# Performance work log

Hardware: AMD Instinct MI355X
Metric: run time of the kernel (lower is better)

Reference implementation:

```python
import jax, jax.numpy as jnp
import numpy as np

V, T, D, H, DK = 16, 2048, 64, 128, 48
LONGEST_GAP, TIME_WINDOW = 144, 48
N_ROLE = 2 * V * V + V


def _run_lengths(md):
    Tn = md.shape[-1]
    m = np.stack((md, md[:, ::-1]), 0).astype(np.int64)
    m[:, :, 0] = 1 - m[:, :, 0]
    for i in range(Tn - 1):
        m[:, :, i + 1] = (1 - m[:, :, i + 1]) * (1 + m[:, :, i])
    return m[0], m[1][:, ::-1].copy()


def _tree_depth_np(mask, times):
    # faithful numpy port of the cached branch of _compute_tree_depth
    Vn, Tn = mask.shape
    time_ind = np.argsort(times, axis=-1)
    time_rev = np.argsort(time_ind, axis=-1)
    mask_depth = np.take_along_axis(mask.astype(np.int64), time_ind, -1)
    current_depth = 1
    max_depth = np.zeros_like(mask_depth)
    prev_mask = np.zeros_like(max_depth)
    next_mask = np.zeros_like(max_depth)
    prev_values = np.zeros_like(max_depth)
    next_values = np.zeros_like(max_depth)
    mask_depth_copy = mask_depth.copy()
    mask_l, mask_r = _run_lengths(mask_depth)
    ci = np.tile(np.arange(Tn), (Vn, 1))
    max_ind = Tn - 1
    while (mask_l + mask_r - 1).max() > LONGEST_GAP:
        centers = mask_l == LONGEST_GAP
        left_ind = mask_l >= LONGEST_GAP
        right_ind = (mask_r + mask_l - 1 >= LONGEST_GAP) & (mask_l <= LONGEST_GAP)
        next_mask[centers] = ((ci + mask_r) > max_ind)[centers].astype(np.int64)
        prev_values[centers] = ci[centers] - mask_l[centers]
        next_values[centers] = (ci[centers] + mask_r[centers]) * (1 - next_mask[centers])
        current_depth += 1
        current_val = mask_l + mask_r
        mask_l[left_ind] -= LONGEST_GAP
        mask_r[right_ind] -= (current_val - LONGEST_GAP)[right_ind]
        mask_r[centers] = 0
        mask_depth_copy[centers] = 1
    mask_depth = mask_depth_copy
    if (1 - mask_depth[:, -1]).sum() > 0 or (1 - mask_depth[:, 0]).sum() > 0:
        end_indices = mask_depth[:, -1] == 0
        start_indices = mask_depth[:, 0] == 0
        prev_mask[:, 0] = start_indices
        next_mask[:, -1] = end_indices
        first_hist = np.arange(Tn, 0, -1)
        last_hist = np.arange(Tn)
        first_hist = np.argmax(first_hist[None, :] * mask_depth, -1)
        last_hist = np.argmax(last_hist[None, :] * mask_depth, -1)
        next_values[start_indices, 0] = first_hist[start_indices]
        prev_values[end_indices, -1] = last_hist[end_indices]
        mask_depth[:, 0] = 1
        mask_depth[:, -1] = 1
        max_depth[end_indices, -1] += current_depth
        max_depth[start_indices, 0] += current_depth
        current_depth += 1
    mask_l, mask_r = _run_lengths(mask_depth)
    while mask_l.sum() > 0:
        half = (mask_l + mask_r) // 2
        centers = (half == mask_l) & (half > 0)
        max_depth[centers] += current_depth
        prev_values[centers] = ci[centers] - mask_l[centers]
        next_values[centers] = ci[centers] + mask_r[centers]
        current_depth += 1
        odd = (mask_l + mask_r + 1) % 2
        s1 = mask_l >= half
        mask_l[s1] -= half[s1]
        s2 = (mask_r > half - odd) & (half > 0)
        mask_r[s2] -= (half - odd)[s2] + 1
    window_indices = ci - TIME_WINDOW
    window_mask = (window_indices < 0) | (window_indices > max_ind)
    window_mask[:, TIME_WINDOW:] |= max_depth[:, TIME_WINDOW:] > max_depth[:, :-TIME_WINDOW]
    window_mask = window_mask.astype(np.int64)
    window_indices = np.clip(window_indices, 0, max_ind)
    max_depth_f = np.take_along_axis(max_depth, time_rev, -1).astype(np.float32)
    next_mask_f = np.take_along_axis(next_mask, time_rev, -1).astype(np.float32)
    prev_mask_f = np.take_along_axis(prev_mask, time_rev, -1).astype(np.float32)
    window_mask_f = np.take_along_axis(window_mask, time_rev, -1).astype(np.float32)
    pv = np.take_along_axis(time_ind, np.clip(prev_values, 0, max_ind), -1)
    pv = np.take_along_axis(pv, time_rev, -1)
    nv = np.take_along_axis(time_ind, np.clip(next_values, 0, max_ind), -1)
    nv = np.take_along_axis(nv, time_rev, -1)
    wi = np.take_along_axis(time_ind, window_indices, -1)
    wi = np.take_along_axis(wi, time_rev, -1)
    offsets = Tn * np.arange(Vn)[:, None]
    indices = np.arange(Tn)[None, :] + offsets
    pv = pv + offsets
    nv = nv + offsets
    wi = wi + offsets
    max_depth_f = max_depth_f + time_ind / 2.0 / (2.0 * Tn)
    return dict(max_depth=max_depth_f, prev_values=pv, next_values=nv, indices=indices,
                prev_mask=prev_mask_f, next_mask=next_mask_f, window_indices=wi,
                window_mask=window_mask_f)


def _mlp(x, W1, b1, W2, b2):
    return jax.nn.relu(x @ W1 + b1) @ W2 + b2


def _forward(encoded, u, Wq1, bq1, Wq2, bq2, Wk1, bk1, Wk2, bk2, Wv1, bv1, Wv2, bv2,
             role_emb, Wd1, bd1, Wd2, bd2, Wm1, bm1, Wm2, bm2,
             prev_values, next_values, window_indices, indices,
             prev_mask, next_mask, window_mask, max_depth):
    Vn, Tn = max_depth.shape
    N = Vn * Tn
    enc = encoded[0].reshape(N, -1)  # [N, D]
    uv = u[0].reshape(N)
    # per-forward depth jitter (torch: max_depth += rand_like/2/(2T))
    md = max_depth + jax.random.uniform(jax.random.key(42), max_depth.shape, max_depth.dtype) / (4.0 * Tn)
    comp = md[:, :, None] > md.T[None]  # [V, T, V]: query deeper than key -> key conditioned on
    pv = jnp.broadcast_to(prev_values.T[None], (Vn, Tn, Vn))
    nv = jnp.where(comp, indices.T[None], next_values.T[None])
    base = Vn * jnp.arange(Vn, dtype=jnp.int32)[:, None] + jnp.arange(Vn, dtype=jnp.int32)[None, :]
    prev_role = jnp.broadcast_to(base[:, None, :], (Vn, Tn, Vn))
    next_role = Vn * Vn + prev_role
    window_role = 2 * Vn * Vn + jnp.broadcast_to(jnp.arange(Vn, dtype=jnp.int32)[:, None, None], (Vn, Tn, 1))
    valid_prev = jnp.broadcast_to((prev_mask.T == 0.0)[None], (Vn, Tn, Vn))
    valid_next = jnp.logical_or(comp, (next_mask.T == 0.0)[None])
    valid_win = (window_mask == 0.0)[:, :, None]
    K = 2 * Vn + 1
    nbr = jnp.concatenate([pv, nv, window_indices[:, :, None]], -1).reshape(N, K)
    roles = jnp.concatenate([prev_role, next_role, window_role], -1).reshape(N, K)
    valid = jnp.concatenate([valid_prev, valid_next, valid_win], -1).reshape(N, K)
    q = _mlp(enc, Wq1, bq1, Wq2, bq2)  # [N, DK]
    k = _mlp(enc, Wk1, bk1, Wk2, bk2)
    v = _mlp(enc, Wv1, bv1, Wv2, bv2)
    keys = k[nbr] + role_emb[roles]  # [N, K, DK] irregular gather
    vals = v[nbr]
    scores = jnp.einsum('nd,nkd->nk', q, keys) / jnp.sqrt(jnp.asarray(q.shape[-1], q.dtype))
    attn = jax.nn.softmax(jnp.where(valid, scores, -1e9), axis=-1)
    ctx = jnp.einsum('nk,nkd->nd', attn, vals)
    dp = _mlp(jnp.concatenate([enc, ctx], -1), Wd1, bd1, Wd2, bd2)  # copula dist params
    mp = _mlp(enc, Wm1, bm1, Wm2, bm2)  # marginal params

    def nlogp(x, mu, log_s):
        s = jax.nn.softplus(log_s) + 1e-3
        z = (x - mu) / s
        return 0.5 * z * z + jnp.log(s) + 0.5 * jnp.log(2.0 * jnp.pi)

    nll = nlogp(uv, dp[:, 0], dp[:, 1]) + nlogp(uv, mp[:, 0], mp[:, 1])
    return nll.reshape(Vn, Tn)


def setup_inputs() -> dict:
    rng = np.random.default_rng(0)
    times = np.sort(rng.uniform(size=(V, T)).astype(np.float32), axis=-1)
    mask = np.zeros((V, T), dtype=bool)
    mask[:, : T // 2] = True  # observed history / prediction gap > longest_gap
    c = _tree_depth_np(mask, times)
    key = jax.random.key(0)
    ks = jax.random.split(key, 13)

    def lin(k, din, dout):
        return jax.random.normal(k, (din, dout), jnp.float32) / np.sqrt(din)

    return {
        'encoded': jax.random.normal(ks[0], (1, V, T, D), jnp.float32),
        'u': jax.random.uniform(ks[1], (1, V, T), jnp.float32),
        'Wq1': lin(ks[2], D, H), 'bq1': jnp.zeros(H, jnp.float32),
        'Wq2': lin(ks[3], H, DK), 'bq2': jnp.zeros(DK, jnp.float32),
        'Wk1': lin(ks[4], D, H), 'bk1': jnp.zeros(H, jnp.float32),
        'Wk2': lin(ks[5], H, DK), 'bk2': jnp.zeros(DK, jnp.float32),
        'Wv1': lin(ks[6], D, H), 'bv1': jnp.zeros(H, jnp.float32),
        'Wv2': lin(ks[7], H, DK), 'bv2': jnp.zeros(DK, jnp.float32),
        'role_emb': 0.02 * jax.random.normal(ks[8], (N_ROLE, DK), jnp.float32),
        'Wd1': lin(ks[9], D + DK, H), 'bd1': jnp.zeros(H, jnp.float32),
        'Wd2': lin(ks[10], H, 2), 'bd2': jnp.zeros(2, jnp.float32),
        'Wm1': lin(ks[11], D, H), 'bm1': jnp.zeros(H, jnp.float32),
        'Wm2': lin(ks[12], H, 2), 'bm2': jnp.zeros(2, jnp.float32),
        'prev_values': jnp.asarray(c['prev_values'], jnp.int32),
        'next_values': jnp.asarray(c['next_values'], jnp.int32),
        'window_indices': jnp.asarray(c['window_indices'], jnp.int32),
        'indices': jnp.asarray(c['indices'], jnp.int32),
        'prev_mask': jnp.asarray(c['prev_mask'], jnp.float32),
        'next_mask': jnp.asarray(c['next_mask'], jnp.float32),
        'window_mask': jnp.asarray(c['window_mask'], jnp.float32),
        'max_depth': jnp.asarray(c['max_depth'], jnp.float32),
    }


def reference(encoded, u, Wq1, bq1, Wq2, bq2, Wk1, bk1, Wk2, bk2, Wv1, bv1, Wv2, bv2,
              role_emb, Wd1, bd1, Wd2, bd2, Wm1, bm1, Wm2, bm2,
              prev_values, next_values, window_indices, indices,
              prev_mask, next_mask, window_mask, max_depth):
    return _forward(encoded, u, Wq1, bq1, Wq2, bq2, Wk1, bk1, Wk2, bk2, Wv1, bv1, Wv2, bv2,
                    role_emb, Wd1, bd1, Wd2, bd2, Wm1, bm1, Wm2, bm2,
                    prev_values, next_values, window_indices, indices,
                    prev_mask, next_mask, window_mask, max_depth)
```

## Files before the change

### kernel.cpp

```cpp
#include <hip/hip_runtime.h>
#include <math.h>

#define VN 16
#define TN 2048
#define NROWS (VN*TN)
#define DIN 64
#define HID 128
#define DKD 48
#define KNB 33
#define BR64 64
#define BRH 32
#define KPAD 52
#define XPAD 68
#define HPAD 66
#define XPADH 36

__device__ __forceinline__ unsigned rotl32(unsigned x, int d){ return (x<<d)|(x>>(32-d)); }

__device__ __forceinline__ void tf2x32(unsigned c0, unsigned c1, unsigned& y0, unsigned& y1){
  const unsigned k0 = 0u, k1 = 42u;
  const unsigned k2 = k0 ^ k1 ^ 0x1BD11BDAu;
  unsigned x0 = c0, x1 = c1;
  x0 += k0; x1 += k1;
#define TF_R(r) { x0 += x1; x1 = rotl32(x1,(r)); x1 ^= x0; }
  TF_R(13) TF_R(15) TF_R(26) TF_R(6)   x0 += k1; x1 += k2 + 1u;
  TF_R(17) TF_R(29) TF_R(16) TF_R(24)  x0 += k2; x1 += k0 + 2u;
  TF_R(13) TF_R(15) TF_R(26) TF_R(6)   x0 += k0; x1 += k1 + 3u;
  TF_R(17) TF_R(29) TF_R(16) TF_R(24)  x0 += k1; x1 += k2 + 4u;
  TF_R(13) TF_R(15) TF_R(26) TF_R(6)   x0 += k2; x1 += k0 + 5u;
#undef TF_R
  y0 = x0; y1 = x1;
}

__device__ __forceinline__ double md64_of(const float* __restrict__ max_depth, int n){
  unsigned y0, y1;
  tf2x32(0u, (unsigned)n, y0, y1);
  unsigned long long bits = (((unsigned long long)y0) << 32) | (unsigned long long)y1;
  unsigned long long fb = (bits >> 12) | 0x3FF0000000000000ull;
  double f; __builtin_memcpy(&f, &fb, 8);
  f -= 1.0;
  return (double)max_depth[n] + f * (1.0/8192.0);
}

__global__ __launch_bounds__(256) void prep_kernel(const float* __restrict__ max_depth,
    const int* __restrict__ pv, const int* __restrict__ nv,
    const float* __restrict__ pm, const float* __restrict__ nm,
    double* __restrict__ mdT, int* __restrict__ pvT, int* __restrict__ nvT,
    float* __restrict__ pmT, float* __restrict__ nmT)
{
  int n = blockIdx.x*256 + threadIdx.x;
  int v = n >> 11, t = n & 2047;
  int o = t*VN + v;
  mdT[o]  = md64_of(max_depth, n);
  pvT[o]  = pv[n];
  nvT[o]  = nv[n];
  pmT[o]  = pm[n];
  nmT[o]  = nm[n];
}

__global__ __launch_bounds__(256) void qkv_kernel(const float* __restrict__ enc,
    const float* __restrict__ Wq1, const float* __restrict__ bq1,
    const float* __restrict__ Wq2, const float* __restrict__ bq2,
    const float* __restrict__ Wk1, const float* __restrict__ bk1,
    const float* __restrict__ Wk2, const float* __restrict__ bk2,
    const float* __restrict__ Wv1, const float* __restrict__ bv1,
    const float* __restrict__ Wv2, const float* __restrict__ bv2,
    float* __restrict__ qo, float* __restrict__ ko, float* __restrict__ vo)
{
  __shared__ __align__(16) float s_x[DIN][XPAD];
  __shared__ __align__(16) float s_h[HID][HPAD];
  int tid = threadIdx.x;
  int mm   = blockIdx.x / 512;
  int base = (blockIdx.x - mm*512) * BR64;

  const float *W1, *b1, *W2, *b2; float* outp;
  if (mm == 0){ W1=Wq1; b1=bq1; W2=Wq2; b2=bq2; outp=qo; }
  else if (mm == 1){ W1=Wk1; b1=bk1; W2=Wk2; b2=bk2; outp=ko; }
  else        { W1=Wv1; b1=bv1; W2=Wv2; b2=bv2; outp=vo; }

  for (int idx = tid; idx < BR64*DIN; idx += 256){
    int r = idx >> 6, c = idx & 63;
    s_x[c][r] = enc[(size_t)(base+r)*DIN + c];
  }
  __syncthreads();

  const int u0 = (tid & 31) * 4;
  const int r0 = (tid >> 5) * 8;
  {
    float acc[8][4];
    float c0=b1[u0], c1=b1[u0+1], c2=b1[u0+2], c3=b1[u0+3];
    #pragma unroll
    for (int r=0;r<8;r++){ acc[r][0]=c0; acc[r][1]=c1; acc[r][2]=c2; acc[r][3]=c3; }
    #pragma unroll 8
    for (int i=0;i<DIN;i++){
      const float4 xa = *reinterpret_cast<const float4*>(&s_x[i][r0]);
      const float4 xb = *reinterpret_cast<const float4*>(&s_x[i][r0+4]);
      const float4 wv = *reinterpret_cast<const float4*>(&W1[i*HID + u0]);
      float xd[8] = {xa.x, xa.y, xa.z, xa.w, xb.x, xb.y, xb.z, xb.w};
      float wd[4] = {wv.x, wv.y, wv.z, wv.w};
      #pragma unroll
      for (int r=0;r<8;r++)
        #pragma unroll
        for (int j=0;j<4;j++)
          acc[r][j] = fmaf(xd[r], wd[j], acc[r][j]);
    }
    #pragma unroll
    for (int j=0;j<4;j++){
      float4 h0, h1;
      h0.x=fmaxf(acc[0][j],0.0f); h0.y=fmaxf(acc[1][j],0.0f);
      h0.z=fmaxf(acc[2][j],0.0f); h0.w=fmaxf(acc[3][j],0.0f);
      h1.x=fmaxf(acc[4][j],0.0f); h1.y=fmaxf(acc[5][j],0.0f);
      h1.z=fmaxf(acc[6][j],0.0f); h1.w=fmaxf(acc[7][j],0.0f);
      *reinterpret_cast<float4*>(&s_h[u0+j][r0])   = h0;
      *reinterpret_cast<float4*>(&s_h[u0+j][r0+4]) = h1;
    }
  }
  __syncthreads();

  const int uo0 = (tid & 15) * 3;
  const int rr0 = (tid >> 4) * 4;
  {
    float a[4][3];
    float c0=b2[uo0], c1=b2[uo0+1], c2=b2[uo0+2];
    #pragma unroll
    for (int r=0;r<4;r++){ a[r][0]=c0; a[r][1]=c1; a[r][2]=c2; }
    #pragma unroll 8
    for (int i=0;i<HID;i++){
      const float4 hv = *reinterpret_cast<const float4*>(&s_h[i][rr0]);
      float w0 = W2[i*DKD+uo0], w1 = W2[i*DKD+uo0+1], w2 = W2[i*DKD+uo0+2];
      float hd[4] = {hv.x, hv.y, hv.z, hv.w};
      #pragma unroll
      for (int r=0;r<4;r++){
        a[r][0]=fmaf(hd[r],w0,a[r][0]);
        a[r][1]=fmaf(hd[r],w1,a[r][1]);
        a[r][2]=fmaf(hd[r],w2,a[r][2]);
      }
    }
    #pragma unroll
    for (int r=0;r<4;r++){
      float* op = outp + (size_t)(base+rr0+r)*DKD;
      op[uo0]=a[r][0]; op[uo0+1]=a[r][1]; op[uo0+2]=a[r][2];
    }
  }
}

__global__ __launch_bounds__(256) void attn_kernel(const float* __restrict__ qv,
    const float* __restrict__ kv, const float* __restrict__ vv,
    const float* __restrict__ role_emb, const double* __restrict__ mdT,
    const int* __restrict__ pvT, const int* __restrict__ nvT,
    const float* __restrict__ pmT, const float* __restrict__ nmT,
    const int* __restrict__ window_indices, const float* __restrict__ window_mask,
    float* __restrict__ ctx_out)
{
  __shared__ __align__(16) float s_role[KNB][KPAD];
  __shared__ __align__(16) float s_q[8][DKD];
  __shared__ float s_p[8][KNB];
  __shared__ int   s_idx[8][KNB];
  int tid  = threadIdx.x;
  int wid  = tid >> 6;
  int lane = tid & 63;
  int nb = blockIdx.x*8;
  int n0 = nb + wid*2;
  int vrow = n0 >> 11;
  int t0   = n0 & 2047;

  for (int idx = tid; idx < 8*DKD; idx += 256){
    int r = idx / DKD, d = idx - r*DKD;
    s_q[r][d] = qv[(size_t)(nb+r)*DKD + d];
  }
  for (int idx = tid; idx < KNB*DKD; idx += 256){
    int j = idx / DKD, d = idx - j*DKD;
    int role = (j < 16) ? (vrow<<4)+j : ((j < 32) ? 256+(vrow<<4)+(j-16) : 512+vrow);
    s_role[j][d] = role_emb[(size_t)role*DKD + d];
  }
  __syncthreads();

  float sc0 = -INFINITY, sc1 = -INFINITY;
  if (lane < KNB){
    int g0, g1; bool va0, va1;
    if (lane < 16){
      int o0 = t0*VN + lane, o1 = o0 + VN;
      g0 = pvT[o0];            g1 = pvT[o1];
      va0 = (pmT[o0] == 0.0f); va1 = (pmT[o1] == 0.0f);
    } else if (lane < 32){
      int v2 = lane - 16;
      int o0 = t0*VN + v2, o1 = o0 + VN;
      bool c0 = mdT[t0*VN + vrow]     > mdT[o0];
      bool c1 = mdT[(t0+1)*VN + vrow] > mdT[o1];
      g0 = c0 ? (v2*TN + t0)     : nvT[o0];
      g1 = c1 ? (v2*TN + t0 + 1) : nvT[o1];
      va0 = c0 || (nmT[o0] == 0.0f);
      va1 = c1 || (nmT[o1] == 0.0f);
    } else {
      g0 = window_indices[n0];   g1 = window_indices[n0+1];
      va0 = (window_mask[n0] == 0.0f); va1 = (window_mask[n0+1] == 0.0f);
    }
    s_idx[wid*2  ][lane] = g0;
    s_idx[wid*2+1][lane] = g1;
    const float4* kp0 = reinterpret_cast<const float4*>(kv + (size_t)g0*DKD);
    const float4* kp1 = reinterpret_cast<const float4*>(kv + (size_t)g1*DKD);
    float a0 = 0.0f, a1 = 0.0f;
    #pragma unroll
    for (int d4 = 0; d4 < DKD/4; d4++){
      const float4 rr = *reinterpret_cast<const float4*>(&s_role[lane][4*d4]);
      const float4 q0 = *reinterpret_cast<const float4*>(&s_q[wid*2  ][4*d4]);
      const float4 q1 = *reinterpret_cast<const float4*>(&s_q[wid*2+1][4*d4]);
      const float4 k0 = kp0[d4];
      const float4 k1 = kp1[d4];
      a0 = fmaf(q0.x, k0.x + rr.x, a0); a1 = fmaf(q1.x, k1.x + rr.x, a1);
      a0 = fmaf(q0.y, k0.y + rr.y, a0); a1 = fmaf(q1.y, k1.y + rr.y, a1);
      a0 = fmaf(q0.z, k0.z + rr.z, a0); a1 = fmaf(q1.z, k1.z + rr.z, a1);
      a0 = fmaf(q0.w, k0.w + rr.w, a0); a1 = fmaf(q1.w, k1.w + rr.w, a1);
    }
    sc0 = a0 / 6.928203230275509f;
    sc1 = a1 / 6.928203230275509f;
    if (!va0) sc0 = -1e9f;
    if (!va1) sc1 = -1e9f;
  }
  float m0 = sc0, m1 = sc1;
  #pragma unroll
  for (int o=32;o>0;o>>=1){
    m0 = fmaxf(m0, __shfl_xor(m0, o, 64));
    m1 = fmaxf(m1, __shfl_xor(m1, o, 64));
  }
  float e0 = (lane < KNB) ? expf(sc0 - m0) : 0.0f;
  float e1 = (lane < KNB) ? expf(sc1 - m1) : 0.0f;
  float s0 = e0, s1 = e1;
  #pragma unroll
  for (int o=32;o>0;o>>=1){
    s0 += __shfl_xor(s0, o, 64);
    s1 += __shfl_xor(s1, o, 64);
  }
  if (lane < KNB){
    s_p[wid*2  ][lane] = e0 / s0;
    s_p[wid*2+1][lane] = e1 / s1;
  }

  if (lane < DKD){
    float c0 = 0.0f, c1 = 0.0f;
    #pragma unroll 8
    for (int j=0;j<KNB;j++){
      int i0 = __builtin_amdgcn_readfirstlane(s_idx[wid*2  ][j]);
      int i1 = __builtin_amdgcn_readfirstlane(s_idx[wid*2+1][j]);
      c0 = fmaf(s_p[wid*2  ][j], vv[(size_t)i0*DKD + lane], c0);
      c1 = fmaf(s_p[wid*2+1][j], vv[(size_t)i1*DKD + lane], c1);
    }
    ctx_out[(size_t)n0*DKD + lane]       = c0;
    ctx_out[(size_t)(n0+1)*DKD + lane]   = c1;
  }
}

__device__ __forceinline__ double nlogp_d(double x, double mu, double ls){
  double sp = fmax(ls, 0.0) + log1p(exp(-fabs(ls)));
  double s = sp + 1e-3;
  double z = (x - mu) / s;
  return 0.5*z*z + log(s) + 0.9189385332046727417803297;
}

__global__ __launch_bounds__(256) void heads_kernel(const float* __restrict__ enc,
    const float* __restrict__ ctx, const float* __restrict__ uu,
    const float* __restrict__ Wd1, const float* __restrict__ bd1,
    const float* __restrict__ Wd2, const float* __restrict__ bd2,
    const float* __restrict__ Wm1, const float* __restrict__ bm1,
    const float* __restrict__ Wm2, const float* __restrict__ bm2,
    float* __restrict__ out)
{
  __shared__ __align__(16) float s_x[DIN+DKD][XPADH];
  __shared__ float s_o[BRH][4];
  int tid = threadIdx.x;
  int base = blockIdx.x * BRH;

  for (int idx = tid; idx < BRH*DIN; idx += 256){
    int r = idx >> 6, c = idx & 63;
    s_x[c][r] = enc[(size_t)(base+r)*DIN + c];
  }
  for (int idx = tid; idx < BRH*DKD; idx += 256){
    int r = idx / DKD, c = idx - r*DKD;
    s_x[DIN + c][r] = ctx[(size_t)(base+r)*DKD + c];
  }
  __syncthreads();

  const int u0 = (tid & 31) * 4;
  const int r0 = (tid >> 5) * 4;

  float pd[4][2] = {{0,0},{0,0},{0,0},{0,0}};
  float pm[4][2] = {{0,0},{0,0},{0,0},{0,0}};

  {
    float acc[4][4];
    float c0=bd1[u0], c1=bd1[u0+1], c2=bd1[u0+2], c3=bd1[u0+3];
    #pragma unroll
    for (int r=0;r<4;r++){ acc[r][0]=c0; acc[r][1]=c1; acc[r][2]=c2; acc[r][3]=c3; }
    #pragma unroll 8
    for (int i=0;i<DIN+DKD;i++){
      const float4 xv = *reinterpret_cast<const float4*>(&s_x[i][r0]);
      const float4 wv = *reinterpret_cast<const float4*>(&Wd1[i*HID + u0]);
      float xd[4] = {xv.x, xv.y, xv.z, xv.w};
      float wd[4] = {wv.x, wv.y, wv.z, wv.w};
      #pragma unroll
      for (int r=0;r<4;r++)
        #pragma unroll
        for (int j=0;j<4;j++)
          acc[r][j] = fmaf(xd[r], wd[j], acc[r][j]);
    }
    #pragma unroll
    for (int j=0;j<4;j++){
      const float2 w2 = *reinterpret_cast<const float2*>(&Wd2[(u0+j)*2]);
      #pragma unroll
      for (int r=0;r<4;r++){
        float h = fmaxf(acc[r][j], 0.0f);
        pd[r][0] = fmaf(h, w2.x, pd[r][0]);
        pd[r][1] = fmaf(h, w2.y, pd[r][1]);
      }
    }
  }
  {
    float acc[4][4];
    float c0=bm1[u0], c1=bm1[u0+1], c2=bm1[u0+2], c3=bm1[u0+3];
    #pragma unroll
    for (int r=0;r<4;r++){ acc[r][0]=c0; acc[r][1]=c1; acc[r][2]=c2; acc[r][3]=c3; }
    #pragma unroll 8
    for (int i=0;i<DIN;i++){
      const float4 xv = *reinterpret_cast<const float4*>(&s_x[i][r0]);
      const float4 wv = *reinterpret_cast<const float4*>(&Wm1[i*HID + u0]);
      float xd[4] = {xv.x, xv.y, xv.z, xv.w};
      float wd[4] = {wv.x, wv.y, wv.z, wv.w};
      #pragma unroll
      for (int r=0;r<4;r++)
        #pragma unroll
        for (int j=0;j<4;j++)
          acc[r][j] = fmaf(xd[r], wd[j], acc[r][j]);
    }
    #pragma unroll
    for (int j=0;j<4;j++){
      const float2 w2 = *reinterpret_cast<const float2*>(&Wm2[(u0+j)*2]);
      #pragma unroll
      for (int r=0;r<4;r++){
        float h = fmaxf(acc[r][j], 0.0f);
        pm[r][0] = fmaf(h, w2.x, pm[r][0]);
        pm[r][1] = fmaf(h, w2.y, pm[r][1]);
      }
    }
  }
  #pragma unroll
  for (int o=1;o<=16;o<<=1){
    #pragma unroll
    for (int r=0;r<4;r++){
      pd[r][0]+=__shfl_xor(pd[r][0],o,64); pd[r][1]+=__shfl_xor(pd[r][1],o,64);
      pm[r][0]+=__shfl_xor(pm[r][0],o,64); pm[r][1]+=__shfl_xor(pm[r][1],o,64);
    }
  }
  if ((tid & 31) == 0){
    #pragma unroll
    for (int r=0;r<4;r++){
      s_o[r0+r][0] = pd[r][0] + bd2[0];
      s_o[r0+r][1] = pd[r][1] + bd2[1];
      s_o[r0+r][2] = pm[r][0] + bm2[0];
      s_o[r0+r][3] = pm[r][1] + bm2[1];
    }
  }
  __syncthreads();

  if (tid < BRH){
    double x = (double)uu[base + tid];
    out[base + tid] = (float)(nlogp_d(x, (double)s_o[tid][0], (double)s_o[tid][1]) +
                              nlogp_d(x, (double)s_o[tid][2], (double)s_o[tid][3]));
  }
}

extern "C" void kernel_launch(void* const* d_in, const int* in_sizes, int n_in,
                              void* d_out, int out_size, void* d_ws, size_t ws_size,
                              hipStream_t stream) {
  const float* encoded = (const float*)d_in[0];
  const float* u       = (const float*)d_in[1];
  const float* Wq1 = (const float*)d_in[2];  const float* bq1 = (const float*)d_in[3];
  const float* Wq2 = (const float*)d_in[4];  const float* bq2 = (const float*)d_in[5];
  const float* Wk1 = (const float*)d_in[6];  const float* bk1 = (const float*)d_in[7];
  const float* Wk2 = (const float*)d_in[8];  const float* bk2 = (const float*)d_in[9];
  const float* Wv1 = (const float*)d_in[10]; const float* bv1 = (const float*)d_in[11];
  const float* Wv2 = (const float*)d_in[12]; const float* bv2 = (const float*)d_in[13];
  const float* role_emb = (const float*)d_in[14];
  const float* Wd1 = (const float*)d_in[15]; const float* bd1 = (const float*)d_in[16];
  const float* Wd2 = (const float*)d_in[17]; const float* bd2 = (const float*)d_in[18];
  const float* Wm1 = (const float*)d_in[19]; const float* bm1 = (const float*)d_in[20];
  const float* Wm2 = (const float*)d_in[21]; const float* bm2 = (const float*)d_in[22];
  const int*   prev_values    = (const int*)d_in[23];
  const int*   next_values    = (const int*)d_in[24];
  const int*   window_indices = (const int*)d_in[25];
  const float* prev_mask   = (const float*)d_in[27];
  const float* next_mask   = (const float*)d_in[28];
  const float* window_mask = (const float*)d_in[29];
  const float* max_depth   = (const float*)d_in[30];
  float* out = (float*)d_out;

  double* mdT = (double*)d_ws;
  float* q  = (float*)(mdT + NROWS);
  float* k  = q  + (size_t)NROWS*DKD;
  float* v  = k  + (size_t)NROWS*DKD;
  float* cx = v  + (size_t)NROWS*DKD;
  int*   pvT  = (int*)(cx + (size_t)NROWS*DKD);
  int*   nvT  = pvT + NROWS;
  float* pmT  = (float*)(nvT + NROWS);
  float* nmT  = pmT + NROWS;

  prep_kernel<<<NROWS/256, 256, 0, stream>>>(max_depth,
      prev_values, next_values, prev_mask, next_mask,
      mdT, pvT, nvT, pmT, nmT);
  qkv_kernel<<<3*(NROWS/BR64), 256, 0, stream>>>(encoded,
      Wq1,bq1,Wq2,bq2, Wk1,bk1,Wk2,bk2, Wv1,bv1,Wv2,bv2, q, k, v);
  attn_kernel<<<NROWS/8, 256, 0, stream>>>(q, k, v, role_emb, mdT,
      pvT, nvT, pmT, nmT, window_indices, window_mask, cx);
  heads_kernel<<<NROWS/BRH, 256, 0, stream>>>(encoded, cx, u,
      Wd1,bd1,Wd2,bd2, Wm1,bm1,Wm2,bm2, out);
}
```

Before: 139.5 us.

## Restructure attention per timestep with shared K/V gather and precomputed role-query scores

Attention now runs one block per timestep covering all 16 vertices. The 64 distinct neighbour K/V rows are gathered once into shared memory and reused across vertices, instead of each row pair independently gathering 33 K and V rows from global memory. The role-embedding dot products q·role are split out into a separate rq_kernel, and window indices and masks are transposed in the prep kernel. This removes redundant global gathers at the cost of an extra kernel launch and an extra intermediate buffer.

Result: no change. 138.5 us (-0.8%).

```diff
diff --git a/kernel.cpp b/kernel.cpp
--- a/kernel.cpp
+++ b/kernel.cpp
@@ -10,10 +10,11 @@
 #define KNB 33
 #define BR64 64
 #define BRH 32
-#define KPAD 52
 #define XPAD 68
 #define HPAD 66
 #define XPADH 36
+#define SPAD 52
+#define RQW 528
 
 __device__ __forceinline__ unsigned rotl32(unsigned x, int d){ return (x<<d)|(x>>(32-d)); }
 
@@ -45,8 +46,10 @@
 __global__ __launch_bounds__(256) void prep_kernel(const float* __restrict__ max_depth,
     const int* __restrict__ pv, const int* __restrict__ nv,
     const float* __restrict__ pm, const float* __restrict__ nm,
+    const int* __restrict__ wi, const float* __restrict__ wm,
     double* __restrict__ mdT, int* __restrict__ pvT, int* __restrict__ nvT,
-    float* __restrict__ pmT, float* __restrict__ nmT)
+    float* __restrict__ pmT, float* __restrict__ nmT,
+    int* __restrict__ wiT, float* __restrict__ wmT)
 {
   int n = blockIdx.x*256 + threadIdx.x;
   int v = n >> 11, t = n & 2047;
@@ -56,6 +59,46 @@
   nvT[o]  = nv[n];
   pmT[o]  = pm[n];
   nmT[o]  = nm[n];
+  wiT[o]  = wi[n];
+  wmT[o]  = wm[n];
+}
+
+__global__ __launch_bounds__(256) void rq_kernel(const float* __restrict__ q,
+    const float* __restrict__ role_emb, float* __restrict__ rqT)
+{
+  __shared__ __align__(16) float s_R[KNB][SPAD];
+  __shared__ __align__(16) float s_Q[64][SPAD];
+  int tid = threadIdx.x;
+  int v  = blockIdx.x >> 5;
+  int tc = blockIdx.x & 31;
+  int t0 = tc*64;
+
+  for (int idx = tid; idx < KNB*DKD; idx += 256){
+    int j = idx / DKD, d = idx - j*DKD;
+    int role = (j<16) ? (v*16+j) : ((j<32) ? 256+v*16+(j-16) : 512+v);
+    s_R[j][d] = role_emb[(size_t)role*DKD + d];
+  }
+  for (int idx = tid; idx < 64*DKD; idx += 256){
+    int r = idx / DKD, d = idx - r*DKD;
+    s_Q[r][d] = q[((size_t)v*TN + t0 + r)*DKD + d];
+  }
+  __syncthreads();
+
+  int r = tid & 63, p = tid >> 6;
+  int t = t0 + r;
+  for (int j = p; j < KNB; j += 4){
+    float acc = 0.0f;
+    #pragma unroll
+    for (int d4=0; d4<12; d4++){
+      const float4 qq = *reinterpret_cast<const float4*>(&s_Q[r][4*d4]);
+      const float4 rr = *reinterpret_cast<const float4*>(&s_R[j][4*d4]);
+      acc = fmaf(qq.x, rr.x, acc);
+      acc = fmaf(qq.y, rr.y, acc);
+      acc = fmaf(qq.z, rr.z, acc);
+      acc = fmaf(qq.w, rr.w, acc);
+    }
+    rqT[(size_t)t*RQW + v*KNB + j] = acc;
+  }
 }
 
 __global__ __launch_bounds__(256) void qkv_kernel(const float* __restrict__ enc,
@@ -146,107 +189,128 @@
 
 __global__ __launch_bounds__(256) void attn_kernel(const float* __restrict__ qv,
     const float* __restrict__ kv, const float* __restrict__ vv,
-    const float* __restrict__ role_emb, const double* __restrict__ mdT,
+    const double* __restrict__ mdT,
     const int* __restrict__ pvT, const int* __restrict__ nvT,
     const float* __restrict__ pmT, const float* __restrict__ nmT,
-    const int* __restrict__ window_indices, const float* __restrict__ window_mask,
+    const int* __restrict__ wiT, const float* __restrict__ wmT,
+    const float* __restrict__ rqT,
     float* __restrict__ ctx_out)
 {
-  __shared__ __align__(16) float s_role[KNB][KPAD];
-  __shared__ __align__(16) float s_q[8][DKD];
-  __shared__ float s_p[8][KNB];
-  __shared__ int   s_idx[8][KNB];
-  int tid  = threadIdx.x;
-  int wid  = tid >> 6;
-  int lane = tid & 63;
-  int nb = blockIdx.x*8;
-  int n0 = nb + wid*2;
-  int vrow = n0 >> 11;
-  int t0   = n0 & 2047;
-
-  for (int idx = tid; idx < 8*DKD; idx += 256){
-    int r = idx / DKD, d = idx - r*DKD;
-    s_q[r][d] = qv[(size_t)(nb+r)*DKD + d];
-  }
-  for (int idx = tid; idx < KNB*DKD; idx += 256){
-    int j = idx / DKD, d = idx - j*DKD;
-    int role = (j < 16) ? (vrow<<4)+j : ((j < 32) ? 256+(vrow<<4)+(j-16) : 512+vrow);
-    s_role[j][d] = role_emb[(size_t)role*DKD + d];
-  }
-  __syncthreads();
-
-  float sc0 = -INFINITY, sc1 = -INFINITY;
-  if (lane < KNB){
-    int g0, g1; bool va0, va1;
-    if (lane < 16){
-      int o0 = t0*VN + lane, o1 = o0 + VN;
-      g0 = pvT[o0];            g1 = pvT[o1];
-      va0 = (pmT[o0] == 0.0f); va1 = (pmT[o1] == 0.0f);
-    } else if (lane < 32){
-      int v2 = lane - 16;
-      int o0 = t0*VN + v2, o1 = o0 + VN;
-      bool c0 = mdT[t0*VN + vrow]     > mdT[o0];
-      bool c1 = mdT[(t0+1)*VN + vrow] > mdT[o1];
-      g0 = c0 ? (v2*TN + t0)     : nvT[o0];
-      g1 = c1 ? (v2*TN + t0 + 1) : nvT[o1];
-      va0 = c0 || (nmT[o0] == 0.0f);
-      va1 = c1 || (nmT[o1] == 0.0f);
-    } else {
-      g0 = window_indices[n0];   g1 = window_indices[n0+1];
-      va0 = (window_mask[n0] == 0.0f); va1 = (window_mask[n0+1] == 0.0f);
-    }
-    s_idx[wid*2  ][lane] = g0;
-    s_idx[wid*2+1][lane] = g1;
-    const float4* kp0 = reinterpret_cast<const float4*>(kv + (size_t)g0*DKD);
-    const float4* kp1 = reinterpret_cast<const float4*>(kv + (size_t)g1*DKD);
-    float a0 = 0.0f, a1 = 0.0f;
-    #pragma unroll
-    for (int d4 = 0; d4 < DKD/4; d4++){
-      const float4 rr = *reinterpret_cast<const float4*>(&s_role[lane][4*d4]);
-      const float4 q0 = *reinterpret_cast<const float4*>(&s_q[wid*2  ][4*d4]);
-      const float4 q1 = *reinterpret_cast<const float4*>(&s_q[wid*2+1][4*d4]);
-      const float4 k0 = kp0[d4];
-      const float4 k1 = kp1[d4];
-      a0 = fmaf(q0.x, k0.x + rr.x, a0); a1 = fmaf(q1.x, k1.x + rr.x, a1);
-      a0 = fmaf(q0.y, k0.y + rr.y, a0); a1 = fmaf(q1.y, k1.y + rr.y, a1);
-      a0 = fmaf(q0.z, k0.z + rr.z, a0); a1 = fmaf(q1.z, k1.z + rr.z, a1);
-      a0 = fmaf(q0.w, k0.w + rr.w, a0); a1 = fmaf(q1.w, k1.w + rr.w, a1);
-    }
-    sc0 = a0 / 6.928203230275509f;
-    sc1 = a1 / 6.928203230275509f;
-    if (!va0) sc0 = -1e9f;
-    if (!va1) sc1 = -1e9f;
-  }
-  float m0 = sc0, m1 = sc1;
+  __shared__ __align__(16) float s_K[64][SPAD];
+  __shared__ __align__(16) float s_V[64][SPAD];
+  __shared__ __align__(16) float s_Q[16][SPAD];
+  __shared__ float s_rq[16][34];
+  __shared__ int    s_g[64];
+  __shared__ double s_md[16];
+  __shared__ float  s_pm[16], s_nm[16], s_wm[16];
+  __shared__ float  s_P1[16][17], s_P2i[16][17], s_P2n[16][17], s_pw[16];
+
+  int tid = threadIdx.x;
+  int t = blockIdx.x;
+  int mbase = t*VN;
+
+  if (tid < 64){
+    int c = tid & 15, g;
+    if (tid < 16)      g = pvT[mbase + c];
+    else if (tid < 32) g = c*TN + t;
+    else if (tid < 48) g = nvT[mbase + c];
+    else               g = wiT[mbase + c];
+    s_g[tid] = g;
+  } else if (tid < 80){
+    s_md[tid-64] = mdT[mbase + (tid-64)];
+  } else if (tid < 96){
+    s_pm[tid-80] = pmT[mbase + (tid-80)];
+  } else if (tid < 112){
+    s_nm[tid-96] = nmT[mbase + (tid-96)];
+  } else if (tid < 128){
+    s_wm[tid-112] = wmT[mbase + (tid-112)];
+  }
+  for (int idx = tid; idx < 16*DKD; idx += 256){
+    int v = idx / DKD, d = idx - v*DKD;
+    s_Q[v][d] = qv[((size_t)v*TN + t)*DKD + d];
+  }
+  for (int idx = tid; idx < RQW; idx += 256){
+    int v = idx / KNB, j = idx - v*KNB;
+    s_rq[v][j] = rqT[(size_t)t*RQW + idx];
+  }
+  __syncthreads();
+  for (int idx = tid; idx < 64*DKD; idx += 256){
+    int slot = idx / DKD, d = idx - slot*DKD;
+    size_t off = (size_t)s_g[slot]*DKD + d;
+    s_K[slot][d] = kv[off];
+    s_V[slot][d] = vv[off];
+  }
+  __syncthreads();
+
+  const int v = tid >> 4, j = tid & 15;
+  float a1=0.f, a2=0.f, a3=0.f;
   #pragma unroll
-  for (int o=32;o>0;o>>=1){
-    m0 = fmaxf(m0, __shfl_xor(m0, o, 64));
-    m1 = fmaxf(m1, __shfl_xor(m1, o, 64));
-  }
-  float e0 = (lane < KNB) ? expf(sc0 - m0) : 0.0f;
-  float e1 = (lane < KNB) ? expf(sc1 - m1) : 0.0f;
-  float s0 = e0, s1 = e1;
+  for (int d4=0; d4<12; d4++){
+    const float4 qq = *reinterpret_cast<const float4*>(&s_Q[v][4*d4]);
+    const float4 kp = *reinterpret_cast<const float4*>(&s_K[j][4*d4]);
+    const float4 ki = *reinterpret_cast<const float4*>(&s_K[16+j][4*d4]);
+    const float4 kn = *reinterpret_cast<const float4*>(&s_K[32+j][4*d4]);
+    a1=fmaf(qq.x,kp.x,a1); a1=fmaf(qq.y,kp.y,a1); a1=fmaf(qq.z,kp.z,a1); a1=fmaf(qq.w,kp.w,a1);
+    a2=fmaf(qq.x,ki.x,a2); a2=fmaf(qq.y,ki.y,a2); a2=fmaf(qq.z,ki.z,a2); a2=fmaf(qq.w,ki.w,a2);
+    a3=fmaf(qq.x,kn.x,a3); a3=fmaf(qq.y,kn.y,a3); a3=fmaf(qq.z,kn.z,a3); a3=fmaf(qq.w,kn.w,a3);
+  }
+  float aw = 0.f;
+  if (j == 0){
+    #pragma unroll
+    for (int d4=0; d4<12; d4++){
+      const float4 qq = *reinterpret_cast<const float4*>(&s_Q[v][4*d4]);
+      const float4 kw = *reinterpret_cast<const float4*>(&s_K[48+v][4*d4]);
+      aw=fmaf(qq.x,kw.x,aw); aw=fmaf(qq.y,kw.y,aw); aw=fmaf(qq.z,kw.z,aw); aw=fmaf(qq.w,kw.w,aw);
+    }
+  }
+  const bool comp = s_md[v] > s_md[j];
+  float scP = (a1 + s_rq[v][j]) / 6.928203230275509f;
+  if (s_pm[j] != 0.0f) scP = -1e9f;
+  float scN = ((comp ? a2 : a3) + s_rq[v][16+j]) / 6.928203230275509f;
+  if (!(comp || s_nm[j] == 0.0f)) scN = -1e9f;
+  float scW = -1e9f;
+  if (j == 0){
+    scW = (aw + s_rq[v][32]) / 6.928203230275509f;
+    if (s_wm[v] != 0.0f) scW = -1e9f;
+  }
+  float m = fmaxf(scP, scN);
+  if (j == 0) m = fmaxf(m, scW);
   #pragma unroll
-  for (int o=32;o>0;o>>=1){
-    s0 += __shfl_xor(s0, o, 64);
-    s1 += __shfl_xor(s1, o, 64);
-  }
-  if (lane < KNB){
-    s_p[wid*2  ][lane] = e0 / s0;
-    s_p[wid*2+1][lane] = e1 / s1;
-  }
-
-  if (lane < DKD){
-    float c0 = 0.0f, c1 = 0.0f;
-    #pragma unroll 8
-    for (int j=0;j<KNB;j++){
-      int i0 = __builtin_amdgcn_readfirstlane(s_idx[wid*2  ][j]);
-      int i1 = __builtin_amdgcn_readfirstlane(s_idx[wid*2+1][j]);
-      c0 = fmaf(s_p[wid*2  ][j], vv[(size_t)i0*DKD + lane], c0);
-      c1 = fmaf(s_p[wid*2+1][j], vv[(size_t)i1*DKD + lane], c1);
-    }
-    ctx_out[(size_t)n0*DKD + lane]       = c0;
-    ctx_out[(size_t)(n0+1)*DKD + lane]   = c1;
+  for (int o=1;o<=8;o<<=1) m = fmaxf(m, __shfl_xor(m, o, 64));
+  float eP = expf(scP - m), eN = expf(scN - m);
+  float eW = (j == 0) ? expf(scW - m) : 0.0f;
+  float S = eP + eN + eW;
+  #pragma unroll
+  for (int o=1;o<=8;o<<=1) S += __shfl_xor(S, o, 64);
+  s_P1 [v][j] = eP / S;
+  s_P2i[v][j] = comp ? (eN / S) : 0.0f;
+  s_P2n[v][j] = comp ? 0.0f : (eN / S);
+  if (j == 0) s_pw[v] = eW / S;
+  __syncthreads();
+
+  if (tid < 192){
+    int pvr = tid / 12, d4 = tid % 12;
+    float4 c; c.x=0.f; c.y=0.f; c.z=0.f; c.w=0.f;
+    #pragma unroll 4
+    for (int jj=0; jj<16; jj++){
+      float p = s_P1[pvr][jj];
+      const float4 vp = *reinterpret_cast<const float4*>(&s_V[jj][4*d4]);
+      c.x=fmaf(p,vp.x,c.x); c.y=fmaf(p,vp.y,c.y); c.z=fmaf(p,vp.z,c.z); c.w=fmaf(p,vp.w,c.w);
+    }
+    #pragma unroll 4
+    for (int jj=0; jj<16; jj++){
+      float pi = s_P2i[pvr][jj], pn = s_P2n[pvr][jj];
+      const float4 vi = *reinterpret_cast<const float4*>(&s_V[16+jj][4*d4]);
+      const float4 vn = *reinterpret_cast<const float4*>(&s_V[32+jj][4*d4]);
+      c.x=fmaf(pi,vi.x,c.x); c.y=fmaf(pi,vi.y,c.y); c.z=fmaf(pi,vi.z,c.z); c.w=fmaf(pi,vi.w,c.w);
+      c.x=fmaf(pn,vn.x,c.x); c.y=fmaf(pn,vn.y,c.y); c.z=fmaf(pn,vn.z,c.z); c.w=fmaf(pn,vn.w,c.w);
+    }
+    {
+      float p = s_pw[pvr];
+      const float4 vw = *reinterpret_cast<const float4*>(&s_V[48+pvr][4*d4]);
+      c.x=fmaf(p,vw.x,c.x); c.y=fmaf(p,vw.y,c.y); c.z=fmaf(p,vw.z,c.z); c.w=fmaf(p,vw.w,c.w);
+    }
+    *reinterpret_cast<float4*>(&ctx_out[((size_t)pvr*TN + t)*DKD + 4*d4]) = c;
   }
 }
 
@@ -402,14 +466,18 @@
   int*   nvT  = pvT + NROWS;
   float* pmT  = (float*)(nvT + NROWS);
   float* nmT  = pmT + NROWS;
+  int*   wiT  = (int*)(nmT + NROWS);
+  float* wmT  = (float*)(wiT + NROWS);
+  float* rqT  = wmT + NROWS;
 
   prep_kernel<<<NROWS/256, 256, 0, stream>>>(max_depth,
-      prev_values, next_values, prev_mask, next_mask,
-      mdT, pvT, nvT, pmT, nmT);
+      prev_values, next_values, prev_mask, next_mask, window_indices, window_mask,
+      mdT, pvT, nvT, pmT, nmT, wiT, wmT);
   qkv_kernel<<<3*(NROWS/BR64), 256, 0, stream>>>(encoded,
       Wq1,bq1,Wq2,bq2, Wk1,bk1,Wk2,bk2, Wv1,bv1,Wv2,bv2, q, k, v);
-  attn_kernel<<<NROWS/8, 256, 0, stream>>>(q, k, v, role_emb, mdT,
-      pvT, nvT, pmT, nmT, window_indices, window_mask, cx);
+  rq_kernel<<<512, 256, 0, stream>>>(q, role_emb, rqT);
+  attn_kernel<<<TN, 256, 0, stream>>>(q, k, v, mdT,
+      pvT, nvT, pmT, nmT, wiT, wmT, rqT, cx);
   heads_kernel<<<NROWS/BRH, 256, 0, stream>>>(encoded, cx, u,
       Wd1,bd1,Wd2,bd2, Wm1,bm1,Wm2,bm2, out);
 }
```
